# Performance work log

Hardware: AMD Instinct MI355X
Metric: run time of the kernel (lower is better)

## Reference

```python
import jax, jax.numpy as jnp
import numpy as np

A = 1000          # nr_assets
LQ = 2048         # len_quote
C = 3             # channels == nr_in
H = 10            # sub_net_out (LSTM hidden)
NLAYER = 3        # hidden_l
HID = A * H       # 10000
MID = HID // 2    # 5000
NPOS = A + 1      # 1001
NOUT = 2001       # nr_out


def lstm_step0(x, w_ih, b_ih, b_hh):
    # One LSTM cell step from zero (h0, c0). w_hh @ h0 == 0 so w_hh drops out
    # of the forward math (it still exists as a parameter). torch gate order i,f,g,o.
    gates = x @ w_ih.T + b_ih + b_hh            # [A, 4H]
    i, f, g, o = jnp.split(gates, 4, axis=-1)
    c = jax.nn.sigmoid(i) * jnp.tanh(g)          # f*c0 == 0
    return jax.nn.sigmoid(o) * jnp.tanh(c)       # [A, H]


def setup_inputs() -> dict:
    key = jax.random.key(0)
    ks = jax.random.split(key, 20)
    s = 0.1
    inp = {
        "quotes": jax.random.normal(ks[0], (A, LQ, C), dtype=jnp.float32),
        "position": jax.random.normal(ks[1], (NPOS,), dtype=jnp.float32),
        # LSTM layer 0 (input C), layers 1,2 (input H)
        "w_ih_l0": s * jax.random.normal(ks[2], (4 * H, C), dtype=jnp.float32),
        "w_hh_l0": s * jax.random.normal(ks[3], (4 * H, H), dtype=jnp.float32),
        "b_ih_l0": s * jax.random.normal(ks[4], (4 * H,), dtype=jnp.float32),
        "b_hh_l0": s * jax.random.normal(ks[5], (4 * H,), dtype=jnp.float32),
        "w_ih_l1": s * jax.random.normal(ks[6], (4 * H, H), dtype=jnp.float32),
        "w_hh_l1": s * jax.random.normal(ks[7], (4 * H, H), dtype=jnp.float32),
        "b_ih_l1": s * jax.random.normal(ks[8], (4 * H,), dtype=jnp.float32),
        "b_hh_l1": s * jax.random.normal(ks[9], (4 * H,), dtype=jnp.float32),
        "w_ih_l2": s * jax.random.normal(ks[10], (4 * H, H), dtype=jnp.float32),
        "w_hh_l2": s * jax.random.normal(ks[11], (4 * H, H), dtype=jnp.float32),
        "b_ih_l2": s * jax.random.normal(ks[12], (4 * H,), dtype=jnp.float32),
        "b_hh_l2": s * jax.random.normal(ks[13], (4 * H,), dtype=jnp.float32),
        "w1": s * jax.random.normal(ks[14], (MID, HID), dtype=jnp.float32),
        "b1": s * jax.random.normal(ks[15], (MID,), dtype=jnp.float32),
        "w2": s * jax.random.normal(ks[16], (NOUT, MID + NPOS), dtype=jnp.float32),
        "b2": s * jax.random.normal(ks[17], (NOUT,), dtype=jnp.float32),
    }
    return inp


def reference(quotes, position,
              w_ih_l0, w_hh_l0, b_ih_l0, b_hh_l0,
              w_ih_l1, w_hh_l1, b_ih_l1, b_hh_l1,
              w_ih_l2, w_hh_l2, b_ih_l2, b_hh_l2,
              w1, b1, w2, b2):
    # Original loop: per-asset quote.view(1, len_quote, C) -> seq_len-1 LSTM with
    # batch=len_quote from zero state; out[:, -1] keeps only the last time row.
    # Equivalent batched form: one 3-layer LSTM cell step on quotes[:, -1, :].
    x = quotes[:, -1, :]                          # [A, C]
    h = lstm_step0(x, w_ih_l0, b_ih_l0, b_hh_l0)  # [A, H]
    h = lstm_step0(h, w_ih_l1, b_ih_l1, b_hh_l1)
    h = lstm_step0(h, w_ih_l2, b_ih_l2, b_hh_l2)
    h = jnp.tanh(h)
    conc = h.reshape(1, -1)                       # concat of [1,H] per asset == [1, A*H]
    lin = jnp.tanh(conc @ w1.T + b1)              # [1, MID]
    out_pos = jnp.concatenate([lin, position.reshape(1, -1)], axis=1)
    return out_pos @ w2.T + b2                    # [1, NOUT]
```

## Files before the change

kernel.cpp:

```cpp
#include <hip/hip_runtime.h>
#include <math.h>

#define A_N    1000
#define LQ_N   2048
#define C_N    3
#define H_N    10
#define HID_N  10000
#define MID_N  5000
#define NPOS_N 1001
#define NOUT_N 2001
#define W2COLS 6001

#define MV1_BLOCKS (MID_N / 4)
#define POS_BLOCKS ((NOUT_N + 3) / 4)
#define B_GRID     (MV1_BLOCKS + POS_BLOCKS)

__device__ __forceinline__ float sigmoidf_(float x) { return 1.0f / (1.0f + expf(-x)); }

__device__ __forceinline__ float wave_reduce(float acc) {
    #pragma unroll
    for (int off = 32; off > 0; off >>= 1) acc += __shfl_down(acc, off, 64);
    return acc;
}

__global__ void __launch_bounds__(256) lstm_head(
    const float* __restrict__ quotes,
    const float* __restrict__ wih0, const float* __restrict__ bih0, const float* __restrict__ bhh0,
    const float* __restrict__ wih1, const float* __restrict__ bih1, const float* __restrict__ bhh1,
    const float* __restrict__ wih2, const float* __restrict__ bih2, const float* __restrict__ bhh2,
    float* __restrict__ conc)
{
    int a = blockIdx.x * blockDim.x + threadIdx.x;
    if (a >= A_N) return;

    const float* q = quotes + (size_t)a * LQ_N * C_N + (size_t)(LQ_N - 1) * C_N;
    float x0 = q[0], x1 = q[1], x2 = q[2];

    float g[40];
    float h[H_N];

    #pragma unroll
    for (int j = 0; j < 40; ++j)
        g[j] = x0 * wih0[j * 3 + 0] + x1 * wih0[j * 3 + 1] + x2 * wih0[j * 3 + 2]
             + bih0[j] + bhh0[j];
    #pragma unroll
    for (int k = 0; k < H_N; ++k) {
        float cc = sigmoidf_(g[k]) * tanhf(g[20 + k]);
        h[k] = sigmoidf_(g[30 + k]) * tanhf(cc);
    }

    #pragma unroll
    for (int j = 0; j < 40; ++j) {
        float s = bih1[j] + bhh1[j];
        #pragma unroll
        for (int k = 0; k < H_N; ++k) s += h[k] * wih1[j * 10 + k];
        g[j] = s;
    }
    float h2[H_N];
    #pragma unroll
    for (int k = 0; k < H_N; ++k) {
        float cc = sigmoidf_(g[k]) * tanhf(g[20 + k]);
        h2[k] = sigmoidf_(g[30 + k]) * tanhf(cc);
    }

    #pragma unroll
    for (int j = 0; j < 40; ++j) {
        float s = bih2[j] + bhh2[j];
        #pragma unroll
        for (int k = 0; k < H_N; ++k) s += h2[k] * wih2[j * 10 + k];
        g[j] = s;
    }
    #pragma unroll
    for (int k = 0; k < H_N; ++k) {
        float cc = sigmoidf_(g[k]) * tanhf(g[20 + k]);
        float hh = sigmoidf_(g[30 + k]) * tanhf(cc);
        conc[a * H_N + k] = tanhf(hh);
    }
}

__global__ void __launch_bounds__(256) fused_mv1_pos(
    const float* __restrict__ w1, const float* __restrict__ b1,
    const float* __restrict__ conc, float* __restrict__ lin,
    const float* __restrict__ w2, const float* __restrict__ b2,
    const float* __restrict__ pos, float* __restrict__ partial)
{
    int lane = threadIdx.x & 63;
    int wid  = threadIdx.x >> 6;

    if (blockIdx.x < MV1_BLOCKS) {
        int row = blockIdx.x * 4 + wid;
        const float4* rb = reinterpret_cast<const float4*>(w1 + (size_t)row * HID_N);
        const float4* v  = reinterpret_cast<const float4*>(conc);
        const int n4 = HID_N / 4;

        float acc0 = 0.0f, acc1 = 0.0f;
        int i = lane;
        for (; i + 64 < n4; i += 128) {
            float4 a0 = rb[i];      float4 c0 = v[i];
            float4 a1 = rb[i + 64]; float4 c1 = v[i + 64];
            acc0 += a0.x * c0.x + a0.y * c0.y + a0.z * c0.z + a0.w * c0.w;
            acc1 += a1.x * c1.x + a1.y * c1.y + a1.z * c1.z + a1.w * c1.w;
        }
        if (i < n4) {
            float4 a = rb[i]; float4 c = v[i];
            acc0 += a.x * c.x + a.y * c.y + a.z * c.z + a.w * c.w;
        }
        float acc = wave_reduce(acc0 + acc1);
        if (lane == 0) lin[row] = tanhf(acc + b1[row]);
    } else {
        int row = (blockIdx.x - MV1_BLOCKS) * 4 + wid;
        if (row >= NOUT_N) return;
        const float* wr = w2 + (size_t)row * W2COLS + MID_N;

        float acc = 0.0f;
        for (int j = lane; j < NPOS_N; j += 64)
            acc += wr[j] * pos[j];
        acc = wave_reduce(acc);
        if (lane == 0) partial[row] = acc + b2[row];
    }
}

__global__ void __launch_bounds__(256) mv2_main(
    const float* __restrict__ w2, const float* __restrict__ lin,
    const float* __restrict__ partial, float* __restrict__ out)
{
    int lane = threadIdx.x & 63;
    int wid  = threadIdx.x >> 6;
    int row  = blockIdx.x * 4 + wid;
    if (row >= NOUT_N) return;

    const float* wr = w2 + (size_t)row * W2COLS;
    const int p = (4 - (row & 3)) & 3;
    const int n    = MID_N - p;
    const int n4   = n >> 2;
    const int tail = n & 3;

    float acc = 0.0f;
    if (lane < p) acc += wr[lane] * lin[lane];

    const float4* rb = reinterpret_cast<const float4*>(wr + p);
    float acc1 = 0.0f;
    int i = lane;
    for (; i + 64 < n4; i += 128) {
        float4 a0 = rb[i];
        float4 a1 = rb[i + 64];
        int j0 = p + 4 * i;
        int j1 = p + 4 * (i + 64);
        acc  += a0.x * lin[j0] + a0.y * lin[j0 + 1] + a0.z * lin[j0 + 2] + a0.w * lin[j0 + 3];
        acc1 += a1.x * lin[j1] + a1.y * lin[j1 + 1] + a1.z * lin[j1 + 2] + a1.w * lin[j1 + 3];
    }
    if (i < n4) {
        float4 a = rb[i];
        int j = p + 4 * i;
        acc += a.x * lin[j] + a.y * lin[j + 1] + a.z * lin[j + 2] + a.w * lin[j + 3];
    }
    if (lane < tail) {
        int j = p + 4 * n4 + lane;
        acc += wr[j] * lin[j];
    }

    float s = wave_reduce(acc + acc1);
    if (lane == 0) out[row] = partial[row] + s;
}

extern "C" void kernel_launch(void* const* d_in, const int* in_sizes, int n_in,
                              void* d_out, int out_size, void* d_ws, size_t ws_size,
                              hipStream_t stream)
{
    const float* quotes = (const float*)d_in[0];
    const float* pos    = (const float*)d_in[1];
    const float* wih0   = (const float*)d_in[2];
    const float* bih0   = (const float*)d_in[4];
    const float* bhh0   = (const float*)d_in[5];
    const float* wih1   = (const float*)d_in[6];
    const float* bih1   = (const float*)d_in[8];
    const float* bhh1   = (const float*)d_in[9];
    const float* wih2   = (const float*)d_in[10];
    const float* bih2   = (const float*)d_in[12];
    const float* bhh2   = (const float*)d_in[13];
    const float* w1     = (const float*)d_in[14];
    const float* b1     = (const float*)d_in[15];
    const float* w2     = (const float*)d_in[16];
    const float* b2     = (const float*)d_in[17];
    float* out = (float*)d_out;

    float* conc    = (float*)d_ws;
    float* lin     = conc + HID_N;
    float* partial = lin + MID_N;

    lstm_head<<<(A_N + 255) / 256, 256, 0, stream>>>(
        quotes, wih0, bih0, bhh0, wih1, bih1, bhh1, wih2, bih2, bhh2, conc);

    fused_mv1_pos<<<B_GRID, 256, 0, stream>>>(
        w1, b1, conc, lin, w2, b2, pos, partial);

    mv2_main<<<POS_BLOCKS, 256, 0, stream>>>(w2, lin, partial, out);
}
```

Before: 69.09 us.

## Move position product into second matvec via concatenated vector, unroll matvec loads

The position vector is copied by an extra LSTM-head block into a concatenated vector following the first-layer output. The second matvec then reads each full w2 row once against that vector, so the separate position partial pass and its buffer are gone. Both matvec kernels now keep four independent float4 loads in flight per iteration with four accumulators. In exchange the w1 bandwidth phase no longer overlaps the position-part reads of w2, so those reads now sit on the critical path after mv1.

```diff
diff --git a/kernel.cpp b/kernel.cpp
--- a/kernel.cpp
+++ b/kernel.cpp
@@ -10,10 +10,7 @@
 #define NPOS_N 1001
 #define NOUT_N 2001
 #define W2COLS 6001
-
-#define MV1_BLOCKS (MID_N / 4)
-#define POS_BLOCKS ((NOUT_N + 3) / 4)
-#define B_GRID     (MV1_BLOCKS + POS_BLOCKS)
+#define VCAT_N 6004
 
 __device__ __forceinline__ float sigmoidf_(float x) { return 1.0f / (1.0f + expf(-x)); }
 
@@ -28,8 +25,16 @@
     const float* __restrict__ wih0, const float* __restrict__ bih0, const float* __restrict__ bhh0,
     const float* __restrict__ wih1, const float* __restrict__ bih1, const float* __restrict__ bhh1,
     const float* __restrict__ wih2, const float* __restrict__ bih2, const float* __restrict__ bhh2,
-    float* __restrict__ conc)
-{
+    const float* __restrict__ pos,
+    float* __restrict__ conc, float* __restrict__ vcat)
+{
+    if (blockIdx.x == 4) {
+        for (int j = threadIdx.x; j < NPOS_N; j += 256)
+            vcat[MID_N + j] = pos[j];
+        if (threadIdx.x < 3) vcat[W2COLS + threadIdx.x] = 0.0f;
+        return;
+    }
+
     int a = blockIdx.x * blockDim.x + threadIdx.x;
     if (a >= A_N) return;
 
@@ -78,51 +83,50 @@
     }
 }
 
-__global__ void __launch_bounds__(256) fused_mv1_pos(
+__global__ void __launch_bounds__(256) mv1(
     const float* __restrict__ w1, const float* __restrict__ b1,
-    const float* __restrict__ conc, float* __restrict__ lin,
-    const float* __restrict__ w2, const float* __restrict__ b2,
-    const float* __restrict__ pos, float* __restrict__ partial)
+    const float* __restrict__ conc, float* __restrict__ vcat)
 {
     int lane = threadIdx.x & 63;
     int wid  = threadIdx.x >> 6;
-
-    if (blockIdx.x < MV1_BLOCKS) {
-        int row = blockIdx.x * 4 + wid;
-        const float4* rb = reinterpret_cast<const float4*>(w1 + (size_t)row * HID_N);
-        const float4* v  = reinterpret_cast<const float4*>(conc);
-        const int n4 = HID_N / 4;
-
-        float acc0 = 0.0f, acc1 = 0.0f;
-        int i = lane;
-        for (; i + 64 < n4; i += 128) {
-            float4 a0 = rb[i];      float4 c0 = v[i];
-            float4 a1 = rb[i + 64]; float4 c1 = v[i + 64];
-            acc0 += a0.x * c0.x + a0.y * c0.y + a0.z * c0.z + a0.w * c0.w;
-            acc1 += a1.x * c1.x + a1.y * c1.y + a1.z * c1.z + a1.w * c1.w;
-        }
-        if (i < n4) {
-            float4 a = rb[i]; float4 c = v[i];
-            acc0 += a.x * c.x + a.y * c.y + a.z * c.z + a.w * c.w;
-        }
-        float acc = wave_reduce(acc0 + acc1);
-        if (lane == 0) lin[row] = tanhf(acc + b1[row]);
-    } else {
-        int row = (blockIdx.x - MV1_BLOCKS) * 4 + wid;
-        if (row >= NOUT_N) return;
-        const float* wr = w2 + (size_t)row * W2COLS + MID_N;
-
-        float acc = 0.0f;
-        for (int j = lane; j < NPOS_N; j += 64)
-            acc += wr[j] * pos[j];
-        acc = wave_reduce(acc);
-        if (lane == 0) partial[row] = acc + b2[row];
-    }
-}
-
-__global__ void __launch_bounds__(256) mv2_main(
-    const float* __restrict__ w2, const float* __restrict__ lin,
-    const float* __restrict__ partial, float* __restrict__ out)
+    int row  = blockIdx.x * 4 + wid;
+
+    const float4* rb = reinterpret_cast<const float4*>(w1 + (size_t)row * HID_N);
+    const float4* cv = reinterpret_cast<const float4*>(conc);
+
+    float acc0 = 0.f, acc1 = 0.f, acc2 = 0.f, acc3 = 0.f;
+    int i = lane;
+    #pragma unroll 1
+    for (int k = 0; k < 9; ++k, i += 256) {
+        float4 a0 = rb[i];       float4 a1 = rb[i + 64];
+        float4 a2 = rb[i + 128]; float4 a3 = rb[i + 192];
+        float4 c0 = cv[i];       float4 c1 = cv[i + 64];
+        float4 c2 = cv[i + 128]; float4 c3 = cv[i + 192];
+        acc0 += a0.x * c0.x + a0.y * c0.y + a0.z * c0.z + a0.w * c0.w;
+        acc1 += a1.x * c1.x + a1.y * c1.y + a1.z * c1.z + a1.w * c1.w;
+        acc2 += a2.x * c2.x + a2.y * c2.y + a2.z * c2.z + a2.w * c2.w;
+        acc3 += a3.x * c3.x + a3.y * c3.y + a3.z * c3.z + a3.w * c3.w;
+    }
+    {
+        float4 a0 = rb[i];       float4 a1 = rb[i + 64];  float4 a2 = rb[i + 128];
+        float4 c0 = cv[i];       float4 c1 = cv[i + 64];  float4 c2 = cv[i + 128];
+        acc0 += a0.x * c0.x + a0.y * c0.y + a0.z * c0.z + a0.w * c0.w;
+        acc1 += a1.x * c1.x + a1.y * c1.y + a1.z * c1.z + a1.w * c1.w;
+        acc2 += a2.x * c2.x + a2.y * c2.y + a2.z * c2.z + a2.w * c2.w;
+    }
+    if (lane < 4) {
+        float4 a = rb[2496 + lane];
+        float4 c = cv[2496 + lane];
+        acc3 += a.x * c.x + a.y * c.y + a.z * c.z + a.w * c.w;
+    }
+
+    float acc = wave_reduce((acc0 + acc1) + (acc2 + acc3));
+    if (lane == 0) vcat[row] = tanhf(acc + b1[row]);
+}
+
+__global__ void __launch_bounds__(256) mv2(
+    const float* __restrict__ w2, const float* __restrict__ b2,
+    const float* __restrict__ vcat, float* __restrict__ out)
 {
     int lane = threadIdx.x & 63;
     int wid  = threadIdx.x >> 6;
@@ -130,37 +134,39 @@
     if (row >= NOUT_N) return;
 
     const float* wr = w2 + (size_t)row * W2COLS;
-    const int p = (4 - (row & 3)) & 3;
-    const int n    = MID_N - p;
+    const int p    = (4 - (row & 3)) & 3;
+    const int n    = W2COLS - p;
     const int n4   = n >> 2;
     const int tail = n & 3;
 
-    float acc = 0.0f;
-    if (lane < p) acc += wr[lane] * lin[lane];
+    float acc0 = 0.f, acc1 = 0.f, acc2 = 0.f, acc3 = 0.f;
+    if (lane < p) acc0 += wr[lane] * vcat[lane];
 
     const float4* rb = reinterpret_cast<const float4*>(wr + p);
-    float acc1 = 0.0f;
     int i = lane;
-    for (; i + 64 < n4; i += 128) {
-        float4 a0 = rb[i];
-        float4 a1 = rb[i + 64];
-        int j0 = p + 4 * i;
-        int j1 = p + 4 * (i + 64);
-        acc  += a0.x * lin[j0] + a0.y * lin[j0 + 1] + a0.z * lin[j0 + 2] + a0.w * lin[j0 + 3];
-        acc1 += a1.x * lin[j1] + a1.y * lin[j1 + 1] + a1.z * lin[j1 + 2] + a1.w * lin[j1 + 3];
-    }
-    if (i < n4) {
+    #pragma unroll 1
+    for (; i + 192 < n4; i += 256) {
+        float4 a0 = rb[i];       float4 a1 = rb[i + 64];
+        float4 a2 = rb[i + 128]; float4 a3 = rb[i + 192];
+        int j0 = p + 4 * i, j1 = j0 + 256, j2 = j0 + 512, j3 = j0 + 768;
+        acc0 += a0.x * vcat[j0] + a0.y * vcat[j0+1] + a0.z * vcat[j0+2] + a0.w * vcat[j0+3];
+        acc1 += a1.x * vcat[j1] + a1.y * vcat[j1+1] + a1.z * vcat[j1+2] + a1.w * vcat[j1+3];
+        acc2 += a2.x * vcat[j2] + a2.y * vcat[j2+1] + a2.z * vcat[j2+2] + a2.w * vcat[j2+3];
+        acc3 += a3.x * vcat[j3] + a3.y * vcat[j3+1] + a3.z * vcat[j3+2] + a3.w * vcat[j3+3];
+    }
+    #pragma unroll 1
+    for (; i < n4; i += 64) {
         float4 a = rb[i];
         int j = p + 4 * i;
-        acc += a.x * lin[j] + a.y * lin[j + 1] + a.z * lin[j + 2] + a.w * lin[j + 3];
+        acc0 += a.x * vcat[j] + a.y * vcat[j+1] + a.z * vcat[j+2] + a.w * vcat[j+3];
     }
     if (lane < tail) {
         int j = p + 4 * n4 + lane;
-        acc += wr[j] * lin[j];
-    }
-
-    float s = wave_reduce(acc + acc1);
-    if (lane == 0) out[row] = partial[row] + s;
+        acc0 += wr[j] * vcat[j];
+    }
+
+    float s = wave_reduce((acc0 + acc1) + (acc2 + acc3));
+    if (lane == 0) out[row] = s + b2[row];
 }
 
 extern "C" void kernel_launch(void* const* d_in, const int* in_sizes, int n_in,
@@ -184,15 +190,14 @@
     const float* b2     = (const float*)d_in[17];
     float* out = (float*)d_out;
 
-    float* conc    = (float*)d_ws;
-    float* lin     = conc + HID_N;
-    float* partial = lin + MID_N;
-
-    lstm_head<<<(A_N + 255) / 256, 256, 0, stream>>>(
-        quotes, wih0, bih0, bhh0, wih1, bih1, bhh1, wih2, bih2, bhh2, conc);
-
-    fused_mv1_pos<<<B_GRID, 256, 0, stream>>>(
-        w1, b1, conc, lin, w2, b2, pos, partial);
-
-    mv2_main<<<POS_BLOCKS, 256, 0, stream>>>(w2, lin, partial, out);
-}
+    float* vcat = (float*)d_ws;
+    float* conc = vcat + 6016;
+
+    lstm_head<<<5, 256, 0, stream>>>(
+        quotes, wih0, bih0, bhh0, wih1, bih1, bhh1, wih2, bih2, bhh2,
+        pos, conc, vcat);
+
+    mv1<<<MID_N / 4, 256, 0, stream>>>(w1, b1, conc, vcat);
+
+    mv2<<<(NOUT_N + 3) / 4, 256, 0, stream>>>(w2, b2, vcat, out);
+}
```

Result: faster. 64.83 us (-6.2%).
